# Kernel optimization log

Hardware: AMD Instinct MI355X
Metric: run time of the kernel (lower is better)

Reference implementation:

```python
import jax, jax.numpy as jnp
import numpy as np

N, K = 16384, 32
SIZE, DIST, SEQ = 128, 32, 16
HEADS, ADIM = 8, 16
HID = 128
E = SIZE + DIST + SEQ
HA = HEADS * ADIM


def _lin(key, fan_in, fan_out):
    kw, kb = jax.random.split(key)
    s = 1.0 / np.sqrt(fan_in)
    W = jax.random.uniform(kw, (fan_in, fan_out), jnp.float32, -s, s)
    b = jax.random.uniform(kb, (fan_out,), jnp.float32, -s, s)
    return W, b


def setup_inputs() -> dict:
    key = jax.random.key(0)
    ks = jax.random.split(key, 12)
    features = jax.random.normal(ks[0], (N, SIZE), jnp.float32)
    distances = jax.random.normal(ks[1], (N, K, DIST), jnp.float32)
    sequence = jax.random.normal(ks[2], (N, K, SEQ), jnp.float32)
    encoder_features = jax.random.normal(ks[3], (N, SIZE), jnp.float32)
    idx = jax.random.randint(ks[4], (N, K), 0, N)
    W1, b1 = _lin(ks[5], SIZE, HID)
    W2, b2 = _lin(ks[6], HID, HID)
    W3, b3 = _lin(ks[7], HID, SIZE)
    Wq, bq = _lin(ks[8], SIZE, HA)
    Wk, bk = _lin(ks[9], E, HA)
    Wv, bv = _lin(ks[10], E, HA)
    Wo, bo = _lin(ks[11], HA, SIZE)
    return dict(features=features, distances=distances, sequence=sequence,
                encoder_features=encoder_features, idx=idx,
                W1=W1, b1=b1, W2=W2, b2=b2, W3=W3, b3=b3,
                Wq=Wq, bq=bq, Wk=Wk, bk=bk, Wv=Wv, bv=bv, Wo=Wo, bo=bo)


def reference(features, distances, sequence, encoder_features, idx,
              W1, b1, W2, b2, W3, b3, Wq, bq, Wk, bk, Wv, bv, Wo, bo):
    # pre-activation + local MLP (depth 3) + activation
    x = jax.nn.relu(features)
    h = jax.nn.relu(x @ W1 + b1)
    h = jax.nn.relu(h @ W2 + b2)
    local = jax.nn.relu(h @ W3 + b3)            # [N, size]
    # edge structure: decoder local + encoder features, gathered at neighbors
    msg = local + encoder_features               # [N, size]
    nb = msg[idx]                                # [N, K, size] irregular gather
    e = jnp.concatenate([nb, distances, sequence], axis=-1)  # [N, K, E]
    # multi-head neighbour dot attention
    q = (features @ Wq + bq).reshape(N, HEADS, ADIM)          # [N, H, A]
    k = (e @ Wk + bk).reshape(N, K, HEADS, ADIM)              # [N, K, H, A]
    v = (e @ Wv + bv).reshape(N, K, HEADS, ADIM)              # [N, K, H, A]
    logits = jnp.einsum('nha,nkha->nkh', q, k) / jnp.sqrt(jnp.float32(ADIM))
    attn = jax.nn.softmax(logits, axis=1)                     # over K
    out = jnp.einsum('nkh,nkha->nha', attn, v).reshape(N, HA)
    attention = out @ Wo + bo                                 # [N, size]
    return features + attention
```

## Files before the change

### kernel.cpp

```cpp
#include <hip/hip_runtime.h>
#include <hip/hip_fp16.h>
#include <math.h>

#define NN 16384
#define TM 32
#define LDA 132
#define LDH 136
#define LDD 36
#define LDS_ 20

typedef unsigned int uint;
typedef unsigned short ushort;
typedef _Float16 half8 __attribute__((ext_vector_type(8)));
typedef float floatx4 __attribute__((ext_vector_type(4)));

__device__ __forceinline__ uint pack2h(float a, float b) {
    _Float16 ha = (_Float16)a, hb = (_Float16)b;
    ushort ua = *(ushort*)&ha, ub = *(ushort*)&hb;
    return (uint)ua | ((uint)ub << 16);
}
__device__ __forceinline__ float2 h2f2(uint u) {
    __half2 h = *(__half2*)&u;
    return __half22float2(h);
}


struct Acc4 { floatx4 a[4]; };

template<bool RELUA>
__device__ __forceinline__ Acc4 mfma_gemm(const ushort* Ab, const half8* wp, int lane, int w)
{
    const int m  = (w & 1) * 16 + (lane & 15);
    const int kq = (lane >> 4) * 8;
    const int cg = w >> 1;
    half8 afr[4];
#pragma unroll
    for (int ks = 0; ks < 4; ++ks) {
        afr[ks] = *(const half8*)&Ab[m * LDH + ks * 32 + kq];
        if (RELUA) {
#pragma unroll
            for (int j = 0; j < 8; ++j)
                afr[ks][j] = afr[ks][j] > (_Float16)0.f ? afr[ks][j] : (_Float16)0.f;
        }
    }
    Acc4 r;
#pragma unroll
    for (int ct = 0; ct < 4; ++ct) {
        const int CT = cg * 4 + ct;
        floatx4 acc = {0.f, 0.f, 0.f, 0.f};
#pragma unroll
        for (int ks = 0; ks < 4; ++ks) {
            half8 bfr = wp[(CT * 4 + ks) * 64 + lane];
            acc = __builtin_amdgcn_mfma_f32_16x16x32_f16(afr[ks], bfr, acc, 0, 0, 0);
        }
        r.a[ct] = acc;
    }
    return r;
}

template<bool HAS_BIAS, bool RELU, bool HAS_ENC, bool F16OUT>
__device__ __forceinline__ void epilogue(const Acc4& ac, const float* __restrict__ bias,
    const float* __restrict__ enc, ushort* dst16, float* dst32,
    int node0, int lane, int w)
{
    const int row0 = (w & 1) * 16 + ((lane >> 4) << 2);
    const int cg = w >> 1;
#pragma unroll
    for (int ct = 0; ct < 4; ++ct) {
        const int col = (cg * 4 + ct) * 16 + (lane & 15);
        float bb = HAS_BIAS ? bias[col] : 0.f;
#pragma unroll
        for (int r = 0; r < 4; ++r) {
            float x = ac.a[ct][r] + bb;
            if (RELU) x = fmaxf(x, 0.f);
            if (HAS_ENC) x += enc[(size_t)(node0 + row0 + r) * 128 + col];
            if (F16OUT) {
                _Float16 h = (_Float16)x;
                dst16[(row0 + r) * LDH + col] = *(ushort*)&h;
            } else {
                dst32[(row0 + r) * LDA + col] = x;
            }
        }
    }
}

__global__ __launch_bounds__(256) void phaseA_kernel(
    const float* __restrict__ features, const float* __restrict__ enc,
    const float* __restrict__ b1, const float* __restrict__ b2,
    const float* __restrict__ b3, const float* __restrict__ bq,
    const float* __restrict__ Wk, const ushort* __restrict__ wpack,
    ushort* __restrict__ qext, ushort* __restrict__ kv)
{
    __shared__ __align__(16) ushort bufA[TM * LDH];
    __shared__ __align__(16) ushort bufB[TM * LDH];
    __shared__ __align__(16) float  qstage[TM * LDA];
    __shared__ __align__(16) float  wk[48 * 128];
    ushort* vstage = (ushort*)qstage;

    const int t = threadIdx.x;
    const int lane = t & 63, w = t >> 6;
    const int node0 = blockIdx.x * TM;

    const half8* wpQ = (const half8*)(wpack + 0 * 16384);
    const half8* wp1 = (const half8*)(wpack + 1 * 16384);
    const half8* wp2 = (const half8*)(wpack + 2 * 16384);
    const half8* wp3 = (const half8*)(wpack + 3 * 16384);
    const half8* wpK = (const half8*)(wpack + 4 * 16384);
    const half8* wpV = (const half8*)(wpack + 5 * 16384);

#pragma unroll
    for (int r = 0; r < 4; ++r) {
        int fid = t + 256 * r;
        int row = fid >> 5, c4 = (fid & 31) * 4;
        float4 v = *(const float4*)&features[(size_t)(node0 + row) * 128 + c4];
        uint2 h = make_uint2(pack2h(v.x, v.y), pack2h(v.z, v.w));
        *(uint2*)&bufA[row * LDH + c4] = h;
    }
#pragma unroll
    for (int r = 0; r < 6; ++r) {
        int fid = t + 256 * r;
        *(float4*)&wk[fid * 4] = *(const float4*)&Wk[128 * 128 + fid * 4];
    }
    __syncthreads();

    Acc4 aQ = mfma_gemm<false>(bufA, wpQ, lane, w);
    Acc4 a1 = mfma_gemm<true >(bufA, wp1, lane, w);
    epilogue<true, false, false, false>(aQ, bq, nullptr, nullptr, qstage, node0, lane, w);
    epilogue<true, true,  false, true >(a1, b1, nullptr, bufB, nullptr, node0, lane, w);
    __syncthreads();

    Acc4 a2 = mfma_gemm<false>(bufB, wp2, lane, w);

    {
        const int m = t >> 3, hh = t & 7;
        float q[16];
#pragma unroll
        for (int jj = 0; jj < 4; ++jj)
            *(float4*)&q[jj * 4] = *(const float4*)&qstage[m * LDA + hh * 16 + jj * 4];
        ushort* dst = &qext[(size_t)(node0 + m) * 512 + hh * 64];
#pragma unroll
        for (int x0 = 0; x0 < 48; x0 += 8) {
            float res[8];
#pragma unroll
            for (int xx = 0; xx < 8; ++xx) {
                const float* wr = &wk[(x0 + xx) * 128 + hh * 16];
                float s = 0.f;
#pragma unroll
                for (int jj = 0; jj < 4; ++jj) {
                    float4 wv = *(const float4*)&wr[jj * 4];
                    s += q[jj*4+0]*wv.x + q[jj*4+1]*wv.y + q[jj*4+2]*wv.z + q[jj*4+3]*wv.w;
                }
                res[xx] = s;
            }
            *(uint4*)&dst[x0] = make_uint4(pack2h(res[0], res[1]), pack2h(res[2], res[3]),
                                           pack2h(res[4], res[5]), pack2h(res[6], res[7]));
        }
        *(uint4*)&dst[48] = make_uint4(pack2h(q[0], q[1]),  pack2h(q[2], q[3]),
                                       pack2h(q[4], q[5]),  pack2h(q[6], q[7]));
        *(uint4*)&dst[56] = make_uint4(pack2h(q[8], q[9]),  pack2h(q[10], q[11]),
                                       pack2h(q[12], q[13]), pack2h(q[14], q[15]));
    }
    epilogue<true, true, false, true>(a2, b2, nullptr, bufA, nullptr, node0, lane, w);
    __syncthreads();

    Acc4 a3 = mfma_gemm<false>(bufA, wp3, lane, w);
    epilogue<true, true, true, true>(a3, b3, enc, bufB, nullptr, node0, lane, w);
    __syncthreads();

    Acc4 aK = mfma_gemm<false>(bufB, wpK, lane, w);
    Acc4 aV = mfma_gemm<false>(bufB, wpV, lane, w);
    epilogue<false, false, false, true>(aK, nullptr, nullptr, bufA,   nullptr, node0, lane, w);
    epilogue<false, false, false, true>(aV, nullptr, nullptr, vstage, nullptr, node0, lane, w);
    __syncthreads();

    {
        int row = t >> 3, c16 = (t & 7) * 16;
        size_t kbase = (size_t)(node0 + row) * 256;
        *(uint4*)&kv[kbase + c16]           = *(const uint4*)&bufA[row * LDH + c16];
        *(uint4*)&kv[kbase + c16 + 8]       = *(const uint4*)&bufA[row * LDH + c16 + 8];
        *(uint4*)&kv[kbase + 128 + c16]     = *(const uint4*)&vstage[row * LDH + c16];
        *(uint4*)&kv[kbase + 128 + c16 + 8] = *(const uint4*)&vstage[row * LDH + c16 + 8];
    }
}

__global__ void wpack_kernel(
    const float* __restrict__ W1, const float* __restrict__ W2,
    const float* __restrict__ W3, const float* __restrict__ Wq,
    const float* __restrict__ Wk, const float* __restrict__ Wv,
    ushort* __restrict__ wpack)
{
    const int g = blockIdx.x >> 5;
    const int rem = blockIdx.x & 31;
    const int CT = rem >> 2, ks = rem & 3;
    const int lane = threadIdx.x;
    const float* W = (g == 0) ? Wq : (g == 1) ? W1 : (g == 2) ? W2
                   : (g == 3) ? W3 : (g == 4) ? Wk : Wv;
    const int n = CT * 16 + (lane & 15);
    const int k0 = ks * 32 + (lane >> 4) * 8;
    ushort out[8];
#pragma unroll
    for (int j = 0; j < 8; ++j) {
        _Float16 h = (_Float16)W[(k0 + j) * 128 + n];
        out[j] = *(ushort*)&h;
    }
    *(uint4*)&wpack[(size_t)(((g * 8 + CT) * 4 + ks) * 64 + lane) * 8] = *(uint4*)out;
}

__global__ __launch_bounds__(256, 6) void attn_kernel(
    const ushort* __restrict__ qext, const ushort* __restrict__ kv,
    const float* __restrict__ dist, const float* __restrict__ seq,
    const int* __restrict__ idx, ushort* __restrict__ ovec)
{
    __shared__ __align__(16) float dists[32 * LDD];
    __shared__ __align__(16) float seqs[32 * LDS_];
    __shared__ __align__(16) float qe[512];
    __shared__ __align__(16) float attn_s[256];
    __shared__ __align__(16) ushort kvv[32 * 128];

    const int t = threadIdx.x;
    const int n = blockIdx.x;
    const int h = t >> 5, k = t & 31;

    int j = idx[n * 32 + k];
    const uint4* mkp = (const uint4*)(kv + (size_t)j * 256 + h * 16);
    uint4 mk0 = mkp[0], mk1 = mkp[1];

    {
        int r = t >> 3, cc = t & 7;
        int j2 = idx[n * 32 + r];
        const uint4* vp = (const uint4*)(kv + (size_t)j2 * 256 + 128 + cc * 16);
        uint4 v0 = vp[0], v1 = vp[1];
        *(uint4*)&kvv[r * 128 + cc * 16] = v0;
        *(uint4*)&kvv[r * 128 + cc * 16 + 8] = v1;
    }
    {
        float4 v = *(const float4*)&dist[(size_t)n * 1024 + t * 4];
        int kk = t >> 3, d0 = (t & 7) * 4;
        *(float4*)&dists[kk * LDD + d0] = v;
    }
    if (t < 128) {
        float4 v = *(const float4*)&seq[(size_t)n * 512 + t * 4];
        int kk = t >> 2, s0 = (t & 3) * 4;
        *(float4*)&seqs[kk * LDS_ + s0] = v;
    }
    if (t < 128) {
        uint4 u = *(const uint4*)&qext[(size_t)n * 512 + t * 8];
        float2 a = h2f2(u.x), b = h2f2(u.y), c = h2f2(u.z), d = h2f2(u.w);
        *(float4*)&qe[t * 8]     = make_float4(a.x, a.y, b.x, b.y);
        *(float4*)&qe[t * 8 + 4] = make_float4(c.x, c.y, d.x, d.y);
    }
    __syncthreads();

    {
        const float* qh = &qe[h * 64 + 48];
        float2 p;
        float lg = 0.f;
        p = h2f2(mk0.x); lg += qh[0]  * p.x + qh[1]  * p.y;
        p = h2f2(mk0.y); lg += qh[2]  * p.x + qh[3]  * p.y;
        p = h2f2(mk0.z); lg += qh[4]  * p.x + qh[5]  * p.y;
        p = h2f2(mk0.w); lg += qh[6]  * p.x + qh[7]  * p.y;
        p = h2f2(mk1.x); lg += qh[8]  * p.x + qh[9]  * p.y;
        p = h2f2(mk1.y); lg += qh[10] * p.x + qh[11] * p.y;
        p = h2f2(mk1.z); lg += qh[12] * p.x + qh[13] * p.y;
        p = h2f2(mk1.w); lg += qh[14] * p.x + qh[15] * p.y;
        const float4* dr = (const float4*)&dists[k * LDD];
        const float4* qd = (const float4*)&qe[h * 64];
#pragma unroll
        for (int i = 0; i < 8; ++i) {
            float4 a = dr[i], b = qd[i];
            lg += a.x * b.x + a.y * b.y + a.z * b.z + a.w * b.w;
        }
        const float4* sr = (const float4*)&seqs[k * LDS_];
        const float4* qs2 = (const float4*)&qe[h * 64 + 32];
#pragma unroll
        for (int i = 0; i < 4; ++i) {
            float4 a = sr[i], b = qs2[i];
            lg += a.x * b.x + a.y * b.y + a.z * b.z + a.w * b.w;
        }
        lg *= 0.25f;
        float mx = lg;
#pragma unroll
        for (int off = 16; off; off >>= 1) mx = fmaxf(mx, __shfl_xor(mx, off));
        float e = __expf(lg - mx);
        float sum = e;
#pragma unroll
        for (int off = 16; off; off >>= 1) sum += __shfl_xor(sum, off);
        attn_s[t] = e / sum;
    }
    __syncthreads();

    ushort* od = &ovec[(size_t)n * 512];
    {
        float wd = 0.f;
#pragma unroll
        for (int i = 0; i < 8; ++i) {
            float4 a = *(const float4*)&attn_s[h * 32 + i * 4];
            wd += a.x * dists[(i * 4 + 0) * LDD + k] + a.y * dists[(i * 4 + 1) * LDD + k]
                + a.z * dists[(i * 4 + 2) * LDD + k] + a.w * dists[(i * 4 + 3) * LDD + k];
        }
        _Float16 hv = (_Float16)wd;
        od[128 + t] = *(ushort*)&hv;
    }
    if (t < 128) {
        const int h2 = t >> 4, s = t & 15;
        float o = 0.f, ws = 0.f;
#pragma unroll
        for (int i = 0; i < 8; ++i) {
            float4 a = *(const float4*)&attn_s[h2 * 32 + i * 4];
            ushort u0 = kvv[(i * 4 + 0) * 128 + t], u1 = kvv[(i * 4 + 1) * 128 + t];
            ushort u2 = kvv[(i * 4 + 2) * 128 + t], u3 = kvv[(i * 4 + 3) * 128 + t];
            o += a.x * __half2float(*(__half*)&u0) + a.y * __half2float(*(__half*)&u1)
               + a.z * __half2float(*(__half*)&u2) + a.w * __half2float(*(__half*)&u3);
            ws += a.x * seqs[(i * 4 + 0) * LDS_ + s] + a.y * seqs[(i * 4 + 1) * LDS_ + s]
                + a.z * seqs[(i * 4 + 2) * LDS_ + s] + a.w * seqs[(i * 4 + 3) * LDS_ + s];
        }
        _Float16 ho = (_Float16)o, hw = (_Float16)ws;
        od[t] = *(ushort*)&ho;
        od[384 + t] = *(ushort*)&hw;
    }
}

__global__ __launch_bounds__(256) void final_kernel(
    const ushort* __restrict__ ovec, const float* __restrict__ BigW,
    const float* __restrict__ cvec, const float* __restrict__ features,
    float* __restrict__ out)
{
    __shared__ __align__(16) float bufA[TM * LDA];
    const int t = threadIdx.x;
    const int node0 = blockIdx.x * TM;
    const int m0 = (t >> 5) * 4;
    const int c0 = (t & 31) * 4;
    float acc[4][4];
#pragma unroll
    for (int mm = 0; mm < 4; ++mm)
#pragma unroll
        for (int cc = 0; cc < 4; ++cc) acc[mm][cc] = 0.f;

    for (int ck = 0; ck < 4; ++ck) {
        __syncthreads();
#pragma unroll
        for (int r = 0; r < 4; ++r) {
            int fid = t + 256 * r;
            int row = fid >> 5, c4 = (fid & 31) * 4;
            uint2 u = *(const uint2*)&ovec[(size_t)(node0 + row) * 512 + ck * 128 + c4];
            float2 a = h2f2(u.x), b = h2f2(u.y);
            *(float4*)&bufA[row * LDA + c4] = make_float4(a.x, a.y, b.x, b.y);
        }
        __syncthreads();
        const float* Wc = BigW + ck * 128 * 128;
#pragma unroll 4
        for (int ic = 0; ic < 32; ++ic) {
            float a[4][4];
#pragma unroll
            for (int mm = 0; mm < 4; ++mm) {
                float4 av = *(const float4*)&bufA[(m0 + mm) * LDA + ic * 4];
                a[mm][0] = av.x; a[mm][1] = av.y; a[mm][2] = av.z; a[mm][3] = av.w;
            }
            float w[4][4];
#pragma unroll
            for (int ii = 0; ii < 4; ++ii) {
                float4 wv = *(const float4*)&Wc[(ic * 4 + ii) * 128 + c0];
                w[ii][0] = wv.x; w[ii][1] = wv.y; w[ii][2] = wv.z; w[ii][3] = wv.w;
            }
#pragma unroll
            for (int mm = 0; mm < 4; ++mm)
#pragma unroll
                for (int ii = 0; ii < 4; ++ii) {
                    float av = a[mm][ii];
#pragma unroll
                    for (int cc = 0; cc < 4; ++cc)
                        acc[mm][cc] = fmaf(av, w[ii][cc], acc[mm][cc]);
                }
        }
    }
    float4 cv = *(const float4*)&cvec[c0];
#pragma unroll
    for (int mm = 0; mm < 4; ++mm) {
        float4 f = *(const float4*)&features[(size_t)(node0 + m0 + mm) * 128 + c0];
        *(float4*)&out[(size_t)(node0 + m0 + mm) * 128 + c0] =
            make_float4(acc[mm][0] + f.x + cv.x, acc[mm][1] + f.y + cv.y,
                        acc[mm][2] + f.z + cv.z, acc[mm][3] + f.w + cv.w);
    }
}

__global__ void wprep_kernel(
    const float* __restrict__ Wv, const float* __restrict__ Wo,
    const float* __restrict__ bv, const float* __restrict__ bo,
    float* __restrict__ BigW, float* __restrict__ cvec)
{
    const int r = blockIdx.x;
    const int c = threadIdx.x;
    float s = 0.f;
    if (r < 128) {
        s = Wo[r * 128 + c];
    } else if (r < 384) {
        int x = r - 128; int hh = x >> 5, d = x & 31;
#pragma unroll
        for (int a = 0; a < 16; ++a)
            s += Wv[(128 + d) * 128 + hh * 16 + a] * Wo[(hh * 16 + a) * 128 + c];
    } else {
        int x = r - 384; int hh = x >> 4, ss = x & 15;
#pragma unroll
        for (int a = 0; a < 16; ++a)
            s += Wv[(160 + ss) * 128 + hh * 16 + a] * Wo[(hh * 16 + a) * 128 + c];
    }
    BigW[r * 128 + c] = s;
    if (r == 0) {
        float cv = bo[c];
        for (int jj = 0; jj < 128; ++jj) cv += bv[jj] * Wo[jj * 128 + c];
        cvec[c] = cv;
    }
}

extern "C" void kernel_launch(void* const* d_in, const int* in_sizes, int n_in,
                              void* d_out, int out_size, void* d_ws, size_t ws_size,
                              hipStream_t stream)
{
    const float* features = (const float*)d_in[0];
    const float* dist     = (const float*)d_in[1];
    const float* seq      = (const float*)d_in[2];
    const float* enc      = (const float*)d_in[3];
    const int*   idx      = (const int*)d_in[4];
    const float* W1 = (const float*)d_in[5];
    const float* b1 = (const float*)d_in[6];
    const float* W2 = (const float*)d_in[7];
    const float* b2 = (const float*)d_in[8];
    const float* W3 = (const float*)d_in[9];
    const float* b3 = (const float*)d_in[10];
    const float* Wq = (const float*)d_in[11];
    const float* bq = (const float*)d_in[12];
    const float* Wk = (const float*)d_in[13];
    const float* Wv = (const float*)d_in[15];
    const float* bv = (const float*)d_in[16];
    const float* Wo = (const float*)d_in[17];
    const float* bo = (const float*)d_in[18];
    float* out = (float*)d_out;

    char* ws = (char*)d_ws;
    ushort* kv    = (ushort*)ws;
    ushort* qext  = (ushort*)(ws + ((size_t)8  << 20));
    ushort* ovec  = (ushort*)(ws + ((size_t)24 << 20));
    float*  BigW  = (float*)(ws + ((size_t)40 << 20));
    float*  cvec  = (float*)(ws + ((size_t)40 << 20) + 262144);
    ushort* wpack = (ushort*)(ws + ((size_t)40 << 20) + 262144 + 512);

    wprep_kernel<<<512, 128, 0, stream>>>(Wv, Wo, bv, bo, BigW, cvec);
    wpack_kernel<<<192, 64, 0, stream>>>(W1, W2, W3, Wq, Wk, Wv, wpack);
    phaseA_kernel<<<NN / TM, 256, 0, stream>>>(
        features, enc, b1, b2, b3, bq, Wk, wpack, qext, kv);
    attn_kernel<<<NN, 256, 0, stream>>>(qext, kv, dist, seq, idx, ovec);
    final_kernel<<<NN / TM, 256, 0, stream>>>(ovec, BigW, cvec, features, out);
}
```

Measured before the change: 271.1 us.

## Store attention staging in fp16 LDS, split seq work, merge weight prep kernels

The attention kernel now stages distances, sequence and the query extension in shared memory as packed fp16 instead of fp32, roughly halving LDS footprint to allow more resident blocks, and computes logits with half2 loads. The weighted-seq output moves to the otherwise idle upper 128 threads so it no longer serialises with the V accumulation. The two weight-preparation kernels are merged into one launch to save launch overhead. Rounding distances and sequence to fp16 adds a little extra precision loss.

```diff
diff --git a/kernel.cpp b/kernel.cpp
--- a/kernel.cpp
+++ b/kernel.cpp
@@ -6,8 +6,8 @@
 #define TM 32
 #define LDA 132
 #define LDH 136
-#define LDD 36
-#define LDS_ 20
+#define LDDH 40
+#define LDSH 24
 
 typedef unsigned int uint;
 typedef unsigned short ushort;
@@ -23,6 +23,13 @@
     __half2 h = *(__half2*)&u;
     return __half22float2(h);
 }
+__device__ __forceinline__ float dot_h2(uint a, uint b, float acc) {
+    __half2 ha = *(__half2*)&a, hb = *(__half2*)&b;
+    acc += (float)__low2half(ha)  * (float)__low2half(hb);
+    acc += (float)__high2half(ha) * (float)__high2half(hb);
+    return acc;
+}
+__device__ __forceinline__ float hval(ushort u) { return (float)*(__half*)&u; }
 
 
 struct Acc4 { floatx4 a[4]; };
@@ -183,27 +190,56 @@
     }
 }
 
-__global__ void wpack_kernel(
+__global__ void prep_kernel(
+    const float* __restrict__ Wv, const float* __restrict__ Wo,
+    const float* __restrict__ bv, const float* __restrict__ bo,
     const float* __restrict__ W1, const float* __restrict__ W2,
     const float* __restrict__ W3, const float* __restrict__ Wq,
-    const float* __restrict__ Wk, const float* __restrict__ Wv,
+    const float* __restrict__ Wk,
+    float* __restrict__ BigW, float* __restrict__ cvec,
     ushort* __restrict__ wpack)
 {
-    const int g = blockIdx.x >> 5;
-    const int rem = blockIdx.x & 31;
-    const int CT = rem >> 2, ks = rem & 3;
-    const int lane = threadIdx.x;
-    const float* W = (g == 0) ? Wq : (g == 1) ? W1 : (g == 2) ? W2
-                   : (g == 3) ? W3 : (g == 4) ? Wk : Wv;
-    const int n = CT * 16 + (lane & 15);
-    const int k0 = ks * 32 + (lane >> 4) * 8;
-    ushort out[8];
-#pragma unroll
-    for (int j = 0; j < 8; ++j) {
-        _Float16 h = (_Float16)W[(k0 + j) * 128 + n];
-        out[j] = *(ushort*)&h;
-    }
-    *(uint4*)&wpack[(size_t)(((g * 8 + CT) * 4 + ks) * 64 + lane) * 8] = *(uint4*)out;
+    const int r = blockIdx.x;
+    const int c = threadIdx.x;
+    if (r < 512) {
+        float s = 0.f;
+        if (r < 128) {
+            s = Wo[r * 128 + c];
+        } else if (r < 384) {
+            int x = r - 128; int hh = x >> 5, d = x & 31;
+#pragma unroll
+            for (int a = 0; a < 16; ++a)
+                s += Wv[(128 + d) * 128 + hh * 16 + a] * Wo[(hh * 16 + a) * 128 + c];
+        } else {
+            int x = r - 384; int hh = x >> 4, ss = x & 15;
+#pragma unroll
+            for (int a = 0; a < 16; ++a)
+                s += Wv[(160 + ss) * 128 + hh * 16 + a] * Wo[(hh * 16 + a) * 128 + c];
+        }
+        BigW[r * 128 + c] = s;
+        if (r == 0) {
+            float cv = bo[c];
+            for (int jj = 0; jj < 128; ++jj) cv += bv[jj] * Wo[jj * 128 + c];
+            cvec[c] = cv;
+        }
+    } else {
+        if (c >= 64) return;
+        const int bb = r - 512;
+        const int g = bb >> 5;
+        const int rem = bb & 31;
+        const int CT = rem >> 2, ks = rem & 3;
+        const float* W = (g == 0) ? Wq : (g == 1) ? W1 : (g == 2) ? W2
+                       : (g == 3) ? W3 : (g == 4) ? Wk : Wv;
+        const int n = CT * 16 + (c & 15);
+        const int k0 = ks * 32 + (c >> 4) * 8;
+        ushort out[8];
+#pragma unroll
+        for (int j = 0; j < 8; ++j) {
+            _Float16 h = (_Float16)W[(k0 + j) * 128 + n];
+            out[j] = *(ushort*)&h;
+        }
+        *(uint4*)&wpack[(size_t)(((g * 8 + CT) * 4 + ks) * 64 + c) * 8] = *(uint4*)out;
+    }
 }
 
 __global__ __launch_bounds__(256, 6) void attn_kernel(
@@ -211,9 +247,9 @@
     const float* __restrict__ dist, const float* __restrict__ seq,
     const int* __restrict__ idx, ushort* __restrict__ ovec)
 {
-    __shared__ __align__(16) float dists[32 * LDD];
-    __shared__ __align__(16) float seqs[32 * LDS_];
-    __shared__ __align__(16) float qe[512];
+    __shared__ __align__(16) ushort distsH[32 * LDDH];
+    __shared__ __align__(16) ushort seqsH[32 * LDSH];
+    __shared__ __align__(16) ushort qeH[512];
     __shared__ __align__(16) float attn_s[256];
     __shared__ __align__(16) ushort kvv[32 * 128];
 
@@ -236,46 +272,40 @@
     {
         float4 v = *(const float4*)&dist[(size_t)n * 1024 + t * 4];
         int kk = t >> 3, d0 = (t & 7) * 4;
-        *(float4*)&dists[kk * LDD + d0] = v;
+        *(uint2*)&distsH[kk * LDDH + d0] = make_uint2(pack2h(v.x, v.y), pack2h(v.z, v.w));
     }
     if (t < 128) {
         float4 v = *(const float4*)&seq[(size_t)n * 512 + t * 4];
         int kk = t >> 2, s0 = (t & 3) * 4;
-        *(float4*)&seqs[kk * LDS_ + s0] = v;
-    }
-    if (t < 128) {
-        uint4 u = *(const uint4*)&qext[(size_t)n * 512 + t * 8];
-        float2 a = h2f2(u.x), b = h2f2(u.y), c = h2f2(u.z), d = h2f2(u.w);
-        *(float4*)&qe[t * 8]     = make_float4(a.x, a.y, b.x, b.y);
-        *(float4*)&qe[t * 8 + 4] = make_float4(c.x, c.y, d.x, d.y);
-    }
-    __syncthreads();
-
-    {
-        const float* qh = &qe[h * 64 + 48];
-        float2 p;
+        *(uint2*)&seqsH[kk * LDSH + s0] = make_uint2(pack2h(v.x, v.y), pack2h(v.z, v.w));
+    }
+    if (t < 64)
+        *(uint4*)&qeH[t * 8] = *(const uint4*)&qext[(size_t)n * 512 + t * 8];
+    __syncthreads();
+
+    {
         float lg = 0.f;
-        p = h2f2(mk0.x); lg += qh[0]  * p.x + qh[1]  * p.y;
-        p = h2f2(mk0.y); lg += qh[2]  * p.x + qh[3]  * p.y;
-        p = h2f2(mk0.z); lg += qh[4]  * p.x + qh[5]  * p.y;
-        p = h2f2(mk0.w); lg += qh[6]  * p.x + qh[7]  * p.y;
-        p = h2f2(mk1.x); lg += qh[8]  * p.x + qh[9]  * p.y;
-        p = h2f2(mk1.y); lg += qh[10] * p.x + qh[11] * p.y;
-        p = h2f2(mk1.z); lg += qh[12] * p.x + qh[13] * p.y;
-        p = h2f2(mk1.w); lg += qh[14] * p.x + qh[15] * p.y;
-        const float4* dr = (const float4*)&dists[k * LDD];
-        const float4* qd = (const float4*)&qe[h * 64];
-#pragma unroll
-        for (int i = 0; i < 8; ++i) {
-            float4 a = dr[i], b = qd[i];
-            lg += a.x * b.x + a.y * b.y + a.z * b.z + a.w * b.w;
-        }
-        const float4* sr = (const float4*)&seqs[k * LDS_];
-        const float4* qs2 = (const float4*)&qe[h * 64 + 32];
+        const uint4* qhp = (const uint4*)&qeH[h * 64 + 48];
+        uint4 q0 = qhp[0], q1 = qhp[1];
+        lg = dot_h2(mk0.x, q0.x, lg); lg = dot_h2(mk0.y, q0.y, lg);
+        lg = dot_h2(mk0.z, q0.z, lg); lg = dot_h2(mk0.w, q0.w, lg);
+        lg = dot_h2(mk1.x, q1.x, lg); lg = dot_h2(mk1.y, q1.y, lg);
+        lg = dot_h2(mk1.z, q1.z, lg); lg = dot_h2(mk1.w, q1.w, lg);
+        const uint4* drp = (const uint4*)&distsH[k * LDDH];
+        const uint4* qdp = (const uint4*)&qeH[h * 64];
 #pragma unroll
         for (int i = 0; i < 4; ++i) {
-            float4 a = sr[i], b = qs2[i];
-            lg += a.x * b.x + a.y * b.y + a.z * b.z + a.w * b.w;
+            uint4 a = drp[i], b = qdp[i];
+            lg = dot_h2(a.x, b.x, lg); lg = dot_h2(a.y, b.y, lg);
+            lg = dot_h2(a.z, b.z, lg); lg = dot_h2(a.w, b.w, lg);
+        }
+        const uint4* srp = (const uint4*)&seqsH[k * LDSH];
+        const uint4* qsp = (const uint4*)&qeH[h * 64 + 32];
+#pragma unroll
+        for (int i = 0; i < 2; ++i) {
+            uint4 a = srp[i], b = qsp[i];
+            lg = dot_h2(a.x, b.x, lg); lg = dot_h2(a.y, b.y, lg);
+            lg = dot_h2(a.z, b.z, lg); lg = dot_h2(a.w, b.w, lg);
         }
         lg *= 0.25f;
         float mx = lg;
@@ -295,28 +325,41 @@
 #pragma unroll
         for (int i = 0; i < 8; ++i) {
             float4 a = *(const float4*)&attn_s[h * 32 + i * 4];
-            wd += a.x * dists[(i * 4 + 0) * LDD + k] + a.y * dists[(i * 4 + 1) * LDD + k]
-                + a.z * dists[(i * 4 + 2) * LDD + k] + a.w * dists[(i * 4 + 3) * LDD + k];
+            wd += a.x * hval(distsH[(i * 4 + 0) * LDDH + k])
+                + a.y * hval(distsH[(i * 4 + 1) * LDDH + k])
+                + a.z * hval(distsH[(i * 4 + 2) * LDDH + k])
+                + a.w * hval(distsH[(i * 4 + 3) * LDDH + k]);
         }
         _Float16 hv = (_Float16)wd;
         od[128 + t] = *(ushort*)&hv;
     }
     if (t < 128) {
-        const int h2 = t >> 4, s = t & 15;
-        float o = 0.f, ws = 0.f;
+        const int h2 = t >> 4;
+        float o = 0.f;
 #pragma unroll
         for (int i = 0; i < 8; ++i) {
             float4 a = *(const float4*)&attn_s[h2 * 32 + i * 4];
-            ushort u0 = kvv[(i * 4 + 0) * 128 + t], u1 = kvv[(i * 4 + 1) * 128 + t];
-            ushort u2 = kvv[(i * 4 + 2) * 128 + t], u3 = kvv[(i * 4 + 3) * 128 + t];
-            o += a.x * __half2float(*(__half*)&u0) + a.y * __half2float(*(__half*)&u1)
-               + a.z * __half2float(*(__half*)&u2) + a.w * __half2float(*(__half*)&u3);
-            ws += a.x * seqs[(i * 4 + 0) * LDS_ + s] + a.y * seqs[(i * 4 + 1) * LDS_ + s]
-                + a.z * seqs[(i * 4 + 2) * LDS_ + s] + a.w * seqs[(i * 4 + 3) * LDS_ + s];
-        }
-        _Float16 ho = (_Float16)o, hw = (_Float16)ws;
+            o += a.x * hval(kvv[(i * 4 + 0) * 128 + t])
+               + a.y * hval(kvv[(i * 4 + 1) * 128 + t])
+               + a.z * hval(kvv[(i * 4 + 2) * 128 + t])
+               + a.w * hval(kvv[(i * 4 + 3) * 128 + t]);
+        }
+        _Float16 ho = (_Float16)o;
         od[t] = *(ushort*)&ho;
-        od[384 + t] = *(ushort*)&hw;
+    } else {
+        const int tt = t - 128;
+        const int h2 = tt >> 4, s = tt & 15;
+        float ws = 0.f;
+#pragma unroll
+        for (int i = 0; i < 8; ++i) {
+            float4 a = *(const float4*)&attn_s[h2 * 32 + i * 4];
+            ws += a.x * hval(seqsH[(i * 4 + 0) * LDSH + s])
+                + a.y * hval(seqsH[(i * 4 + 1) * LDSH + s])
+                + a.z * hval(seqsH[(i * 4 + 2) * LDSH + s])
+                + a.w * hval(seqsH[(i * 4 + 3) * LDSH + s]);
+        }
+        _Float16 hw = (_Float16)ws;
+        od[384 + tt] = *(ushort*)&hw;
     }
 }
 
@@ -380,35 +423,6 @@
         *(float4*)&out[(size_t)(node0 + m0 + mm) * 128 + c0] =
             make_float4(acc[mm][0] + f.x + cv.x, acc[mm][1] + f.y + cv.y,
                         acc[mm][2] + f.z + cv.z, acc[mm][3] + f.w + cv.w);
-    }
-}
-
-__global__ void wprep_kernel(
-    const float* __restrict__ Wv, const float* __restrict__ Wo,
-    const float* __restrict__ bv, const float* __restrict__ bo,
-    float* __restrict__ BigW, float* __restrict__ cvec)
-{
-    const int r = blockIdx.x;
-    const int c = threadIdx.x;
-    float s = 0.f;
-    if (r < 128) {
-        s = Wo[r * 128 + c];
-    } else if (r < 384) {
-        int x = r - 128; int hh = x >> 5, d = x & 31;
-#pragma unroll
-        for (int a = 0; a < 16; ++a)
-            s += Wv[(128 + d) * 128 + hh * 16 + a] * Wo[(hh * 16 + a) * 128 + c];
-    } else {
-        int x = r - 384; int hh = x >> 4, ss = x & 15;
-#pragma unroll
-        for (int a = 0; a < 16; ++a)
-            s += Wv[(160 + ss) * 128 + hh * 16 + a] * Wo[(hh * 16 + a) * 128 + c];
-    }
-    BigW[r * 128 + c] = s;
-    if (r == 0) {
-        float cv = bo[c];
-        for (int jj = 0; jj < 128; ++jj) cv += bv[jj] * Wo[jj * 128 + c];
-        cvec[c] = cv;
     }
 }
 
@@ -444,8 +458,8 @@
     float*  cvec  = (float*)(ws + ((size_t)40 << 20) + 262144);
     ushort* wpack = (ushort*)(ws + ((size_t)40 << 20) + 262144 + 512);
 
-    wprep_kernel<<<512, 128, 0, stream>>>(Wv, Wo, bv, bo, BigW, cvec);
-    wpack_kernel<<<192, 64, 0, stream>>>(W1, W2, W3, Wq, Wk, Wv, wpack);
+    prep_kernel<<<704, 128, 0, stream>>>(Wv, Wo, bv, bo, W1, W2, W3, Wq, Wk,
+                                         BigW, cvec, wpack);
     phaseA_kernel<<<NN / TM, 256, 0, stream>>>(
         features, enc, b1, b2, b3, bq, Wk, wpack, qext, kv);
     attn_kernel<<<NN, 256, 0, stream>>>(qext, kv, dist, seq, idx, ovec);
```

After: 267.1 us. Within noise of the previous version (-1.5%).
